# Kernel optimization log

Measured on AMD Instinct MI355X. Metric: run time of the kernel, lower is better.

The kernel has to match this reference:

```python
import jax, jax.numpy as jnp
import numpy as np

B, SEQ, DIM = 2, 2048, 1024
HEADS, HEAD_DIM = 16, 64
HIDDEN = 2816
EPS = 1e-5
LN_EPS = 1e-5


def rmsnorm(x, w, eps=EPS):
    return x * jax.lax.rsqrt(jnp.mean(x * x, axis=-1, keepdims=True) + eps) * w


def layernorm(x, w, b, eps=LN_EPS):
    mu = jnp.mean(x, axis=-1, keepdims=True)
    var = jnp.mean((x - mu) ** 2, axis=-1, keepdims=True)
    return (x - mu) * jax.lax.rsqrt(var + eps) * w + b


def modulate(x, shift, scale):
    # x: [B,S,D], shift/scale: [B,D]
    return x * (1.0 + scale[:, None, :]) + shift[:, None, :]


def apply_rope(t, cos, sin):
    # t: [B,S,H,D]; cos/sin: [S, D/2] -> complex multiply on (even,odd) pairs
    t = t.reshape(*t.shape[:-1], HEAD_DIM // 2, 2)
    t0, t1 = t[..., 0], t[..., 1]
    c = cos[None, :, None, :]
    s = sin[None, :, None, :]
    o0 = t0 * c - t1 * s
    o1 = t0 * s + t1 * c
    return jnp.stack([o0, o1], axis=-1).reshape(*t.shape[:-2], HEAD_DIM)


def setup_inputs() -> dict:
    key = jax.random.key(0)
    ks = jax.random.split(key, 12)
    def w(k, shape, s=0.02):
        return jax.random.normal(k, shape, dtype=jnp.float32) * s
    x = jax.random.normal(ks[0], (B, SEQ, DIM), dtype=jnp.float32)
    adaln_input = jax.random.normal(ks[1], (B, DIM), dtype=jnp.float32)
    pos = jnp.arange(SEQ, dtype=jnp.float32)
    inv_freq = 1.0 / (10000.0 ** (jnp.arange(0, HEAD_DIM, 2, dtype=jnp.float32) / HEAD_DIM))
    ang = pos[:, None] * inv_freq[None, :]  # [S, D/2]
    return dict(
        x=x, adaln_input=adaln_input,
        freqs_cos=jnp.cos(ang), freqs_sin=jnp.sin(ang),
        wq=w(ks[2], (DIM, DIM)), wk=w(ks[3], (DIM, DIM)),
        wv=w(ks[4], (DIM, DIM)), wo=w(ks[5], (DIM, DIM)),
        q_norm_w=jnp.ones(DIM, jnp.float32), q_norm_b=jnp.zeros(DIM, jnp.float32),
        k_norm_w=jnp.ones(DIM, jnp.float32), k_norm_b=jnp.zeros(DIM, jnp.float32),
        attn_norm_w=jnp.ones(DIM, jnp.float32), ffn_norm_w=jnp.ones(DIM, jnp.float32),
        ada_w=w(ks[6], (DIM, 6 * DIM)), ada_b=jnp.zeros(6 * DIM, jnp.float32),
        w1=w(ks[7], (DIM, HIDDEN)), w2=w(ks[8], (HIDDEN, DIM)), w3=w(ks[9], (DIM, HIDDEN)),
    )


def reference(x, adaln_input, freqs_cos, freqs_sin, wq, wk, wv, wo,
              q_norm_w, q_norm_b, k_norm_w, k_norm_b,
              attn_norm_w, ffn_norm_w, ada_w, ada_b, w1, w2, w3):
    # adaLN modulation: SiLU -> Linear -> 6 chunks of [B, DIM]
    m = jax.nn.silu(adaln_input) @ ada_w + ada_b
    shift_msa, scale_msa, gate_msa, shift_mlp, scale_mlp, gate_mlp = jnp.split(m, 6, axis=1)

    # --- attention branch ---
    h = modulate(rmsnorm(x, attn_norm_w), shift_msa, scale_msa)
    xq = layernorm(h @ wq, q_norm_w, q_norm_b)
    xk = layernorm(h @ wk, k_norm_w, k_norm_b)
    xv = h @ wv
    xq = xq.reshape(B, SEQ, HEADS, HEAD_DIM)
    xk = xk.reshape(B, SEQ, HEADS, HEAD_DIM)
    xv = xv.reshape(B, SEQ, HEADS, HEAD_DIM)
    xq = apply_rope(xq, freqs_cos, freqs_sin)
    xk = apply_rope(xk, freqs_cos, freqs_sin)
    scale = 1.0 / jnp.sqrt(jnp.float32(HEAD_DIM))
    scores = jnp.einsum('bshd,bthd->bhst', xq, xk) * scale  # [B,H,S,S]
    probs = jax.nn.softmax(scores, axis=-1)
    attn = jnp.einsum('bhst,bthd->bshd', probs, xv).reshape(B, SEQ, DIM)
    attn = attn @ wo
    x = x + gate_msa[:, None, :] * attn

    # --- MLP branch (SwiGLU) ---
    h = modulate(rmsnorm(x, ffn_norm_w), shift_mlp, scale_mlp)
    ffn = (jax.nn.silu(h @ w1) * (h @ w3)) @ w2
    x = x + gate_mlp[:, None, :] * ffn
    return x
```

## Files before the change

### kernel.cpp

```cpp
#include <hip/hip_runtime.h>
#include <hip/hip_bf16.h>

#define B_   2
#define S_   2048
#define D_   1024
#define H_   16
#define HD_  64
#define HID_ 2816

typedef unsigned short u16;
typedef unsigned int   u32;
typedef __attribute__((ext_vector_type(8))) short short8;
typedef __attribute__((ext_vector_type(4))) float f32x4;
typedef __attribute__((ext_vector_type(4))) u32   u32x4;

static __device__ __forceinline__ float bf2f(u16 u){ return __uint_as_float(((u32)u)<<16); }
static __device__ __forceinline__ u16 f2bf(float f){
  u32 u = __float_as_uint(f);
  u32 r = (u + 0x7FFFu + ((u>>16)&1u)) >> 16;
  return (u16)r;
}
static __device__ __forceinline__ u16 f2bfr(float f){
  return (u16)((__float_as_uint(f) + 0x8000u) >> 16);
}
static __device__ __forceinline__ u32 pk2(float a, float b){
  return ((__float_as_uint(a) + 0x8000u) >> 16) | ((__float_as_uint(b) + 0x8000u) & 0xFFFF0000u);
}

static __device__ __forceinline__ void ld4(const u16* p, float* v){
  ushort4 t = *reinterpret_cast<const ushort4*>(p);
  v[0]=bf2f(t.x); v[1]=bf2f(t.y); v[2]=bf2f(t.z); v[3]=bf2f(t.w);
}
static __device__ __forceinline__ void ld4(const float* p, float* v){
  float4 t = *reinterpret_cast<const float4*>(p);
  v[0]=t.x; v[1]=t.y; v[2]=t.z; v[3]=t.w;
}
static __device__ __forceinline__ void st4(u16* p, const float* v){
  ushort4 t; t.x=f2bf(v[0]); t.y=f2bf(v[1]); t.z=f2bf(v[2]); t.w=f2bf(v[3]);
  *reinterpret_cast<ushort4*>(p)=t;
}

static __device__ __forceinline__ float ld1g(const void* p, size_t i, bool f32){
  return f32 ? ((const float*)p)[i] : bf2f(((const u16*)p)[i]);
}
static __device__ __forceinline__ void ld4g(const void* p, size_t i, float* v, bool f32){
  if(f32){
    float4 t = *reinterpret_cast<const float4*>((const float*)p + i);
    v[0]=t.x; v[1]=t.y; v[2]=t.z; v[3]=t.w;
  }else{
    ushort4 t = *reinterpret_cast<const ushort4*>((const u16*)p + i);
    v[0]=bf2f(t.x); v[1]=bf2f(t.y); v[2]=bf2f(t.z); v[3]=bf2f(t.w);
  }
}
static __device__ __forceinline__ void st4g(void* p, size_t i, const float* v, bool f32){
  if(f32){
    float4 t; t.x=v[0]; t.y=v[1]; t.z=v[2]; t.w=v[3];
    *reinterpret_cast<float4*>((float*)p + i) = t;
  }else{
    st4((u16*)p + i, v);
  }
}

static __device__ __forceinline__ void gl2lds16(const u16* g, const u16* l){
  typedef __attribute__((address_space(3))) u16 lds_u16;
  typedef const __attribute__((address_space(1))) u16 glb_u16;
  __builtin_amdgcn_global_load_lds((glb_u16*)(uintptr_t)g,
                                   (lds_u16*)(u32)(uintptr_t)l, 16, 0, 0);
}

__global__ __launch_bounds__(256) void k_probe_zero(const u16* fc_raw, int* flag, float* m){
  int i = blockIdx.x*256 + threadIdx.x;
  if(i < 12288) m[i] = 0.f;
  if(i == 0) *flag = (fc_raw[0]==0) ? 1 : 0;
}

static __device__ __forceinline__ float blk_sum(float v, float* red){
  #pragma unroll
  for(int o=32;o;o>>=1) v += __shfl_xor(v,o,64);
  int lane = threadIdx.x & 63, w = threadIdx.x >> 6;
  if(lane==0) red[w]=v;
  __syncthreads();
  float t = red[0]+red[1]+red[2]+red[3];
  __syncthreads();
  return t;
}

__global__ __launch_bounds__(256) void k_adaln(const void* a, const void* W, const void* bias,
                                               float* m, const int* flag){
  bool f32 = flag[0] != 0;
  __shared__ float sl[2][128];
  int bk = blockIdx.y;
  {
    int bb = threadIdx.x >> 7, kk = threadIdx.x & 127;
    float x = ld1g(a, bb*D_ + bk*128 + kk, f32);
    sl[bb][kk] = x/(1.f+__expf(-x));
  }
  __syncthreads();
  int n = blockIdx.x*256 + threadIdx.x;
  float p0 = 0.f, p1 = 0.f;
  for(int kk=0;kk<128;kk++){
    float w = ld1g(W, (size_t)(bk*128+kk)*6144 + n, f32);
    p0 += sl[0][kk]*w; p1 += sl[1][kk]*w;
  }
  if(bk==0){ float bv = ld1g(bias, n, f32); p0 += bv; p1 += bv; }
  atomicAdd(&m[n], p0);
  atomicAdd(&m[6144+n], p1);
}

__global__ __launch_bounds__(256) void k_rms_mod(const void* x, const void* nw, const float* m,
                                                 u16* h, int shift_off, int scale_off,
                                                 const int* flag){
  bool f32 = flag[0] != 0;
  __shared__ float red[4];
  int row = blockIdx.x; int b = row >> 11;
  int d0 = threadIdx.x*4;
  float v[4]; ld4g(x, (size_t)row*D_ + d0, v, f32);
  float ss = v[0]*v[0]+v[1]*v[1]+v[2]*v[2]+v[3]*v[3];
  float tot = blk_sum(ss, red);
  float r = rsqrtf(tot*(1.f/D_) + 1e-5f);
  const float* mb = m + b*6144;
  float wn[4]; ld4g(nw, d0, wn, f32);
  float o[4];
  #pragma unroll
  for(int j=0;j<4;j++){
    int d = d0+j;
    o[j] = v[j]*r*wn[j]*(1.f+mb[scale_off+d]) + mb[shift_off+d];
  }
  st4(h + (size_t)row*D_ + d0, o);
}

__global__ __launch_bounds__(256) void k_resid_rms(const void* x, const u16* y, const float* m,
                                                   const void* nw, float* x2, u16* h,
                                                   const int* flag){
  bool f32 = flag[0] != 0;
  __shared__ float red[4];
  int row = blockIdx.x; int b = row >> 11;
  int d0 = threadIdx.x*4;
  size_t i4 = (size_t)row*D_ + d0;
  float xv[4], yv[4];
  ld4g(x, i4, xv, f32); ld4(y+i4, yv);
  const float* mb = m + b*6144;
  float v[4];
  #pragma unroll
  for(int j=0;j<4;j++) v[j] = xv[j] + mb[2048+d0+j]*yv[j];
  float4 t; t.x=v[0]; t.y=v[1]; t.z=v[2]; t.w=v[3];
  *reinterpret_cast<float4*>(x2+i4) = t;
  float ss = v[0]*v[0]+v[1]*v[1]+v[2]*v[2]+v[3]*v[3];
  float tot = blk_sum(ss, red);
  float r = rsqrtf(tot*(1.f/D_) + 1e-5f);
  float wn[4]; ld4g(nw, d0, wn, f32);
  float o[4];
  #pragma unroll
  for(int j=0;j<4;j++)
    o[j] = v[j]*r*wn[j]*(1.f+mb[4096+d0+j]) + mb[3072+d0+j];
  st4(h + i4, o);
}

__global__ __launch_bounds__(256) void k_ln_rope2(u16* t, const void* qw, const void* qb,
                                                  const void* kw, const void* kb2,
                                                  const void* fc, const void* fs, const int* flag){
  bool f32 = flag[0] != 0;
  __shared__ float red[4];
  int row = blockIdx.x; int s = row & (S_-1);
  const void* w  = blockIdx.y ? kw  : qw;
  const void* bb = blockIdx.y ? kb2 : qb;
  int d0 = threadIdx.x*4;
  u16* tp = t + (size_t)row*3072 + blockIdx.y*1024 + d0;
  float v[4]; ld4(tp, v);
  float sm = v[0]+v[1]+v[2]+v[3];
  float sq = v[0]*v[0]+v[1]*v[1]+v[2]*v[2]+v[3]*v[3];
  float tsm = blk_sum(sm, red);
  float tsq = blk_sum(sq, red);
  float mu  = tsm*(1.f/D_);
  float var = tsq*(1.f/D_) - mu*mu;
  float rs  = rsqrtf(var + 1e-5f);
  float wv[4], bv[4]; ld4g(w, d0, wv, f32); ld4g(bb, d0, bv, f32);
  float y[4];
  #pragma unroll
  for(int j=0;j<4;j++) y[j] = (v[j]-mu)*rs*wv[j] + bv[j];
  int pos = d0 & 63; int i0 = pos>>1;
  float c0 = ld1g(fc, s*32+i0,   f32), s0 = ld1g(fs, s*32+i0,   f32);
  float c1 = ld1g(fc, s*32+i0+1, f32), s1 = ld1g(fs, s*32+i0+1, f32);
  float o[4];
  o[0] = y[0]*c0 - y[1]*s0;
  o[1] = y[0]*s0 + y[1]*c0;
  o[2] = y[2]*c1 - y[3]*s1;
  o[3] = y[2]*s1 + y[3]*c1;
  st4(tp, o);
}

__global__ __launch_bounds__(256) void k_wt3(const void* W0, const void* W1, const void* W2,
                                             u16* WT, int Kd, int Nd, const int* flag){
  bool f32 = flag[0] != 0;
  const void* W = blockIdx.z==0 ? W0 : (blockIdx.z==1 ? W1 : W2);
  u16* dst_base = WT + (size_t)blockIdx.z * (size_t)Kd * Nd;
  __shared__ u16 L[64][72];
  int tid = threadIdx.x;
  int k0 = blockIdx.x*64, n0 = blockIdx.y*64;
  int r = tid>>2, c0 = (tid&3)*16;
  if(f32){
    const float* Wf = (const float*)W;
    #pragma unroll
    for(int j=0;j<4;j++){
      float4 t = *reinterpret_cast<const float4*>(&Wf[(size_t)(k0+r)*Nd + n0 + c0 + j*4]);
      L[r][c0+j*4+0]=f2bfr(t.x); L[r][c0+j*4+1]=f2bfr(t.y);
      L[r][c0+j*4+2]=f2bfr(t.z); L[r][c0+j*4+3]=f2bfr(t.w);
    }
  }else{
    const u16* Wh = (const u16*)W;
    *reinterpret_cast<short8*>(&L[r][c0]) =
      *reinterpret_cast<const short8*>(&Wh[(size_t)(k0+r)*Nd + n0 + c0]);
    *reinterpret_cast<short8*>(&L[r][c0+8]) =
      *reinterpret_cast<const short8*>(&Wh[(size_t)(k0+r)*Nd + n0 + c0 + 8]);
  }
  __syncthreads();
  int n = tid>>2, kk0 = (tid&3)*16;
  u16 tmp[16];
  #pragma unroll
  for(int j=0;j<16;j++) tmp[j] = L[kk0+j][n];
  u16* dst = dst_base + (size_t)(n0+n)*Kd + k0 + kk0;
  *reinterpret_cast<short8*>(dst)   = *reinterpret_cast<const short8*>(tmp);
  *reinterpret_cast<short8*>(dst+8) = *reinterpret_cast<const short8*>(tmp+8);
}

template<int TM>
__global__ __launch_bounds__(256) void k_gemm_mfma(const u16* A, int lda, const u16* BT, int ldb,
                                                   u16* C, int M, int N, int K){
  __shared__ __align__(16) u16 As[TM*64];
  __shared__ __align__(16) u16 Bs[128*64];
  int tid = threadIdx.x, lane = tid&63, w = tid>>6;
  int col = lane&15, quad = lane>>4;
  int row0 = blockIdx.y*TM, col0 = blockIdx.x*128;
  const u16* Ab = A  + (size_t)row0*lda;
  const u16* Bb = BT + (size_t)col0*ldb;
  constexpr int MI = TM/32;
  int wm = (w>>1)*(TM/2);
  int wn = (w&1)*64;
  f32x4 acc[MI][4];
  #pragma unroll
  for(int i=0;i<MI;i++)
    #pragma unroll
    for(int j=0;j<4;j++) acc[i][j] = (f32x4){0.f,0.f,0.f,0.f};

  for(int k0=0;k0<K;k0+=64){
    __syncthreads();
    #pragma unroll
    for(int i=0;i<TM/32;i++){
      int c = i*256 + w*64 + lane;
      int r = c>>3, s = c&7, gs = s ^ (r&7);
      gl2lds16(Ab + (size_t)r*lda + k0 + gs*8, As + (size_t)c*8);
    }
    #pragma unroll
    for(int i=0;i<4;i++){
      int c = i*256 + w*64 + lane;
      int r = c>>3, s = c&7, gs = s ^ (r&7);
      gl2lds16(Bb + (size_t)r*ldb + k0 + gs*8, Bs + (size_t)c*8);
    }
    __syncthreads();
    #pragma unroll
    for(int ks=0;ks<64;ks+=32){
      short8 af[MI], bfr[4];
      #pragma unroll
      for(int mi=0;mi<MI;mi++){
        int r = wm+mi*16+col;
        int sch = ((ks>>3) + quad) ^ (col&7);
        af[mi] = *reinterpret_cast<const short8*>(&As[r*64 + sch*8]);
      }
      #pragma unroll
      for(int ni=0;ni<4;ni++){
        int r = wn+ni*16+col;
        int sch = ((ks>>3) + quad) ^ (col&7);
        bfr[ni] = *reinterpret_cast<const short8*>(&Bs[r*64 + sch*8]);
      }
      #pragma unroll
      for(int mi=0;mi<MI;mi++)
        #pragma unroll
        for(int ni=0;ni<4;ni++)
          acc[mi][ni] = __builtin_amdgcn_mfma_f32_16x16x32_bf16(af[mi], bfr[ni], acc[mi][ni], 0,0,0);
    }
  }
  #pragma unroll
  for(int mi=0;mi<MI;mi++)
    #pragma unroll
    for(int r=0;r<4;r++){
      size_t rowoff = (size_t)(row0+wm+mi*16+quad*4+r)*N + col0 + wn;
      #pragma unroll
      for(int ni=0;ni<4;ni++)
        C[rowoff + ni*16 + col] = f2bfr(acc[mi][ni][r]);
    }
}

__global__ __launch_bounds__(256) void k_vt(const u16* v, int vstr, u16* vt){
  __shared__ u16 L[64][72];
  int tid = threadIdx.x;
  int wg = blockIdx.x;
  int kblk = wg & 31; int bh = wg >> 5; int h = bh & 15, b = bh >> 4;
  int row = tid>>2, c0 = (tid&3)*16;
  const u16* src = v + (size_t)(b*S_ + kblk*64 + row)*vstr + h*HD_ + c0;
  *reinterpret_cast<short8*>(&L[row][c0])   = *reinterpret_cast<const short8*>(src);
  *reinterpret_cast<short8*>(&L[row][c0+8]) = *reinterpret_cast<const short8*>(src+8);
  __syncthreads();
  int hd = tid>>2, k0 = (tid&3)*16;
  u16 tmp[16];
  #pragma unroll
  for(int j=0;j<16;j++) tmp[j] = L[k0+j][hd];
  u16* dst = vt + ((size_t)bh*HD_ + hd)*S_ + kblk*64 + k0;
  *reinterpret_cast<short8*>(dst)   = *reinterpret_cast<const short8*>(tmp);
  *reinterpret_cast<short8*>(dst+8) = *reinterpret_cast<const short8*>(tmp+8);
}

__global__ __launch_bounds__(256) void k_attn_mfma(const u16* q, const u16* k, const u16* vt,
                                                   u16* o, int qks){
  __shared__ __align__(16) u16 Ks[64*88];
  __shared__ __align__(16) u16 Vs[64*88];
  int tid = threadIdx.x, lane = tid & 63, wid = tid >> 6;
  int col = lane & 15, quad = lane >> 4;
  int wg = blockIdx.x;
  int qblk = wg & 31; int bh = wg >> 5; int h = bh & 15, b = bh >> 4;

  const u16* kb  = k  + (size_t)b*S_*qks + h*HD_;
  const u16* vtb = vt + (size_t)bh*HD_*S_;

  short8 qa0, qa1;
  {
    const float qscale = 0.18033688f;
    const u16* qp = q + (size_t)(b*S_ + qblk*64 + wid*16 + col)*qks + h*HD_ + quad*8;
    short8 t0 = *reinterpret_cast<const short8*>(qp);
    short8 t1 = *reinterpret_cast<const short8*>(qp + 32);
    #pragma unroll
    for(int j=0;j<8;j++){
      qa0[j] = (short)f2bf(bf2f((u16)t0[j])*qscale);
      qa1[j] = (short)f2bf(bf2f((u16)t1[j])*qscale);
    }
  }
  float m_i = -1e30f, l_i = 0.f;
  f32x4 acc[4];
  #pragma unroll
  for(int t=0;t<4;t++) acc[t] = (f32x4){0.f,0.f,0.f,0.f};

  const u16 *kp[2]; const u16 *vp[2]; u16 *ksd[2], *vsd[2];
  #pragma unroll
  for(int g=0;g<2;g++){
    int c = g*256 + tid;
    int l = c>>3, kc = (c&7)*8;
    int kl = 32*(l>>5) + 8*((l>>2)&3) + 4*((l>>4)&1) + (l&3);
    kp[g]  = kb + (size_t)kl*qks + kc;
    vp[g]  = vtb + (size_t)l*S_ + kc;
    ksd[g] = Ks + l*88 + kc;
    vsd[g] = Vs + l*88 + kc;
  }

  for(int t0=0;t0<S_;t0+=64){
    __syncthreads();
    #pragma unroll
    for(int g=0;g<2;g++){
      *reinterpret_cast<short8*>(ksd[g]) =
        *reinterpret_cast<const short8*>(kp[g] + (size_t)t0*qks);
      *reinterpret_cast<short8*>(vsd[g]) =
        *reinterpret_cast<const short8*>(vp[g] + t0);
    }
    __syncthreads();

    f32x4 st[4];
    #pragma unroll
    for(int mt=0;mt<4;mt++){
      st[mt] = (f32x4){0.f,0.f,0.f,0.f};
      short8 ka0 = *reinterpret_cast<const short8*>(&Ks[(mt*16+col)*88 + quad*8]);
      short8 ka1 = *reinterpret_cast<const short8*>(&Ks[(mt*16+col)*88 + 32 + quad*8]);
      st[mt] = __builtin_amdgcn_mfma_f32_16x16x32_bf16(ka0, qa0, st[mt], 0,0,0);
      st[mt] = __builtin_amdgcn_mfma_f32_16x16x32_bf16(ka1, qa1, st[mt], 0,0,0);
    }
    float cm = st[0][0];
    #pragma unroll
    for(int mt=0;mt<4;mt++)
      #pragma unroll
      for(int r=0;r<4;r++) cm = fmaxf(cm, st[mt][r]);
    cm = fmaxf(cm, __shfl_xor(cm,16,64));
    cm = fmaxf(cm, __shfl_xor(cm,32,64));
    float mn = fmaxf(m_i, cm);
    float al = __builtin_amdgcn_exp2f(m_i - mn);
    m_i = mn;
    float pe[4][4];
    #pragma unroll
    for(int mt=0;mt<4;mt++)
      #pragma unroll
      for(int r=0;r<4;r++) pe[mt][r] = __builtin_amdgcn_exp2f(st[mt][r]-mn);
    #pragma unroll
    for(int t=0;t<4;t++) acc[t] *= al;
    #pragma unroll
    for(int w=0;w<2;w++){
      u32x4 pw;
      pw[0] = pk2(pe[2*w][0],   pe[2*w][1]);
      pw[1] = pk2(pe[2*w][2],   pe[2*w][3]);
      pw[2] = pk2(pe[2*w+1][0], pe[2*w+1][1]);
      pw[3] = pk2(pe[2*w+1][2], pe[2*w+1][3]);
      short8 pb = *reinterpret_cast<short8*>(&pw);
      #pragma unroll
      for(int ht=0;ht<4;ht++){
        short8 vf = *reinterpret_cast<const short8*>(&Vs[(ht*16+col)*88 + w*32 + quad*8]);
        acc[ht] = __builtin_amdgcn_mfma_f32_16x16x32_bf16(vf, pb, acc[ht], 0,0,0);
      }
    }
    float ps = 0.f;
    #pragma unroll
    for(int mt=0;mt<4;mt++)
      #pragma unroll
      for(int r=0;r<4;r++) ps += pe[mt][r];
    ps += __shfl_xor(ps,16,64);
    ps += __shfl_xor(ps,32,64);
    l_i = l_i*al + ps;
  }
  float inv = __builtin_amdgcn_rcpf(l_i);
  u16* ob = o + (size_t)(b*S_ + qblk*64 + wid*16 + col)*D_ + h*HD_;
  #pragma unroll
  for(int ht=0;ht<4;ht++){
    uint2 t;
    t.x = pk2(acc[ht][0]*inv, acc[ht][1]*inv);
    t.y = pk2(acc[ht][2]*inv, acc[ht][3]*inv);
    *reinterpret_cast<uint2*>(ob + ht*16 + quad*4) = t;
  }
}

__global__ __launch_bounds__(256) void k_resid_b(const float* x, const u16* y, const float* m,
                                                 int gate_off, void* o, const int* flag){
  bool f32 = flag[0] != 0;
  size_t i4 = ((size_t)blockIdx.x*256 + threadIdx.x)*4;
  int d = (int)(i4 & (D_-1));
  int b = (int)(i4 >> 21);
  float xv[4], yv[4];
  ld4(x+i4, xv); ld4(y+i4, yv);
  const float* g = m + b*6144 + gate_off + d;
  float r[4];
  #pragma unroll
  for(int j=0;j<4;j++) r[j] = xv[j] + g[j]*yv[j];
  st4g(o, i4, r, f32);
}

__global__ __launch_bounds__(256) void k_silu_mul(u16* h13){
  int c4 = (blockIdx.x*256 + threadIdx.x)*4;
  if(c4 >= HID_) return;
  u16* p = h13 + (size_t)blockIdx.y*5632 + c4;
  float a[4], c[4];
  ld4(p, a); ld4(p + HID_, c);
  float r[4];
  #pragma unroll
  for(int j=0;j<4;j++){ float sv = a[j]/(1.f+__expf(-a[j])); r[j] = sv*c[j]; }
  st4(p, r);
}

extern "C" void kernel_launch(void* const* d_in, const int* in_sizes, int n_in,
                              void* d_out, int out_size, void* d_ws, size_t ws_size,
                              hipStream_t stream){
  const void* x   = d_in[0];
  const void* ada = d_in[1];
  const void* fc  = d_in[2];
  const void* fs  = d_in[3];
  const void* wq  = d_in[4];
  const void* wk  = d_in[5];
  const void* wv  = d_in[6];
  const void* wo  = d_in[7];
  const void* qnw = d_in[8];
  const void* qnb = d_in[9];
  const void* knw = d_in[10];
  const void* knb = d_in[11];
  const void* anw = d_in[12];
  const void* fnw = d_in[13];
  const void* aw  = d_in[14];
  const void* ab  = d_in[15];
  const void* w1  = d_in[16];
  const void* w2  = d_in[17];
  const void* w3  = d_in[18];
  char* ws = (char*)d_ws;
  const size_t MB = 1u<<20;

  int*   flag = (int*)ws;
  float* m    = (float*)(ws + 4096);
  u16*  hbuf  = (u16*)(ws + 1*MB);
  u16*  xqkv  = (u16*)(ws + 9*MB);
  float* x2   = (float*)(ws + 9*MB);
  u16*  proj  = (u16*)(ws + 25*MB);
  u16*  wreg  = (u16*)(ws + 33*MB);
  u16*  h13   = (u16*)(ws + 45*MB);
  u16*  vt    = wreg;

  dim3 blk(256);

  k_probe_zero<<<dim3(48), blk, 0, stream>>>((const u16*)fc, flag, m);
  k_adaln<<<dim3(24,8), blk, 0, stream>>>(ada, aw, ab, m, flag);
  k_rms_mod<<<dim3(B_*S_), blk, 0, stream>>>(x, anw, m, hbuf, 0, 1024, flag);

  k_wt3<<<dim3(16,16,3), blk, 0, stream>>>(wq, wk, wv, wreg, 1024, 1024, flag);
  k_gemm_mfma<128><<<dim3(24,32), blk, 0, stream>>>(hbuf, 1024, wreg, 1024, xqkv, 4096, 3072, 1024);

  k_ln_rope2<<<dim3(B_*S_,2), blk, 0, stream>>>(xqkv, qnw, qnb, knw, knb, fc, fs, flag);
  k_vt<<<dim3(B_*H_*S_/64), blk, 0, stream>>>(xqkv + 2048, 3072, vt);
  k_attn_mfma<<<dim3(B_*H_*S_/64), blk, 0, stream>>>(xqkv, xqkv + 1024, vt, hbuf, 3072);

  k_wt3<<<dim3(16,16,1), blk, 0, stream>>>(wo, wo, wo, wreg, 1024, 1024, flag);
  k_gemm_mfma<64><<<dim3(8,64), blk, 0, stream>>>(hbuf, 1024, wreg, 1024, proj, 4096, 1024, 1024);
  k_resid_rms<<<dim3(B_*S_), blk, 0, stream>>>(x, proj, m, fnw, x2, hbuf, flag);

  k_wt3<<<dim3(16,44,2), blk, 0, stream>>>(w1, w3, w3, wreg, 1024, 2816, flag);
  k_gemm_mfma<128><<<dim3(44,32), blk, 0, stream>>>(hbuf, 1024, wreg, 1024, h13, 4096, 5632, 1024);
  k_silu_mul<<<dim3(3,4096), blk, 0, stream>>>(h13);
  k_wt3<<<dim3(44,16,1), blk, 0, stream>>>(w2, w2, w2, wreg, 2816, 1024, flag);
  k_gemm_mfma<64><<<dim3(8,64), blk, 0, stream>>>(h13, 5632, wreg, 2816, proj, 4096, 1024, 2816);
  k_resid_b<<<dim3(4096), blk, 0, stream>>>(x2, proj, m, 5120, d_out, flag);
}
```

Baseline: 457.1 us.

## Fuse SwiGLU and residual into GEMM epilogues, double-buffer attention K/V tiles

The w1/w3 weights are now interleaved in 32-column groups so each GEMM tile holds matching gate and up columns, and the SiLU-multiply runs in the GEMM epilogue. That removes the separate silu_mul kernel and halves the intermediate writes. The final w2 GEMM now applies the gated residual directly in its epilogue, replacing k_resid_b and the proj round-trip. Attention gains double-buffered K/V shared tiles with register prefetch, a smaller row stride, and rescaling that is skipped when the running max is unchanged, which adds a warp-uniform branch.

Measured after the change: 441.8 us. -3.4%, faster.

```diff
diff --git a/kernel.cpp b/kernel.cpp
--- a/kernel.cpp
+++ b/kernel.cpp
@@ -223,9 +223,48 @@
   *reinterpret_cast<short8*>(dst+8) = *reinterpret_cast<const short8*>(tmp+8);
 }
 
-template<int TM>
+__global__ __launch_bounds__(256) void k_wt13(const void* W1, const void* W3,
+                                              u16* WT, const int* flag){
+  bool f32 = flag[0] != 0;
+  const int Kd = 1024, Nd = HID_;
+  const void* W = blockIdx.z ? W3 : W1;
+  int radd = blockIdx.z ? 32 : 0;
+  __shared__ u16 L[64][72];
+  int tid = threadIdx.x;
+  int k0 = blockIdx.x*64, n0 = blockIdx.y*64;
+  int r = tid>>2, c0 = (tid&3)*16;
+  if(f32){
+    const float* Wf = (const float*)W;
+    #pragma unroll
+    for(int j=0;j<4;j++){
+      float4 t = *reinterpret_cast<const float4*>(&Wf[(size_t)(k0+r)*Nd + n0 + c0 + j*4]);
+      L[r][c0+j*4+0]=f2bfr(t.x); L[r][c0+j*4+1]=f2bfr(t.y);
+      L[r][c0+j*4+2]=f2bfr(t.z); L[r][c0+j*4+3]=f2bfr(t.w);
+    }
+  }else{
+    const u16* Wh = (const u16*)W;
+    *reinterpret_cast<short8*>(&L[r][c0]) =
+      *reinterpret_cast<const short8*>(&Wh[(size_t)(k0+r)*Nd + n0 + c0]);
+    *reinterpret_cast<short8*>(&L[r][c0+8]) =
+      *reinterpret_cast<const short8*>(&Wh[(size_t)(k0+r)*Nd + n0 + c0 + 8]);
+  }
+  __syncthreads();
+  int n = tid>>2, kk0 = (tid&3)*16;
+  u16 tmp[16];
+  #pragma unroll
+  for(int j=0;j<16;j++) tmp[j] = L[kk0+j][n];
+  int nglob = n0 + n;
+  int rw = ((nglob>>5)<<6) + (nglob&31) + radd;
+  u16* dst = WT + (size_t)rw*Kd + k0 + kk0;
+  *reinterpret_cast<short8*>(dst)   = *reinterpret_cast<const short8*>(tmp);
+  *reinterpret_cast<short8*>(dst+8) = *reinterpret_cast<const short8*>(tmp+8);
+}
+
+template<int TM, int EPI>
 __global__ __launch_bounds__(256) void k_gemm_mfma(const u16* A, int lda, const u16* BT, int ldb,
-                                                   u16* C, int M, int N, int K){
+                                                   u16* C, int N, int K,
+                                                   const float* x2, const float* mg,
+                                                   void* outp, const int* flag){
   __shared__ __align__(16) u16 As[TM*64];
   __shared__ __align__(16) u16 Bs[128*64];
   int tid = threadIdx.x, lane = tid&63, w = tid>>6;
@@ -279,15 +318,48 @@
           acc[mi][ni] = __builtin_amdgcn_mfma_f32_16x16x32_bf16(af[mi], bfr[ni], acc[mi][ni], 0,0,0);
     }
   }
-  #pragma unroll
-  for(int mi=0;mi<MI;mi++)
-    #pragma unroll
-    for(int r=0;r<4;r++){
-      size_t rowoff = (size_t)(row0+wm+mi*16+quad*4+r)*N + col0 + wn;
-      #pragma unroll
-      for(int ni=0;ni<4;ni++)
-        C[rowoff + ni*16 + col] = f2bfr(acc[mi][ni][r]);
-    }
+  if constexpr(EPI==0){
+    #pragma unroll
+    for(int mi=0;mi<MI;mi++)
+      #pragma unroll
+      for(int r=0;r<4;r++){
+        size_t rowoff = (size_t)(row0+wm+mi*16+quad*4+r)*N + col0 + wn;
+        #pragma unroll
+        for(int ni=0;ni<4;ni++)
+          C[rowoff + ni*16 + col] = f2bfr(acc[mi][ni][r]);
+      }
+  } else if constexpr(EPI==1){
+    int cb = blockIdx.x*64 + (wn?32:0) + col;
+    #pragma unroll
+    for(int mi=0;mi<MI;mi++)
+      #pragma unroll
+      for(int r=0;r<4;r++){
+        int row = row0+wm+mi*16+quad*4+r;
+        u16* gp = C + (size_t)row*HID_ + cb;
+        #pragma unroll
+        for(int ni=0;ni<2;ni++){
+          float a = acc[mi][ni][r], cc = acc[mi][ni+2][r];
+          float sv = a * __builtin_amdgcn_rcpf(1.f + __builtin_amdgcn_exp2f(-1.4426950f*a));
+          gp[ni*16] = f2bfr(sv*cc);
+        }
+      }
+  } else {
+    bool f32o = flag[0] != 0;
+    #pragma unroll
+    for(int mi=0;mi<MI;mi++)
+      #pragma unroll
+      for(int r=0;r<4;r++){
+        int row = row0+wm+mi*16+quad*4+r;
+        int b = row >> 11;
+        #pragma unroll
+        for(int ni=0;ni<4;ni++){
+          int cc = col0 + wn + ni*16 + col;
+          float v = x2[(size_t)row*D_ + cc] + mg[b*6144 + 5120 + cc]*acc[mi][ni][r];
+          if(f32o) ((float*)outp)[(size_t)row*D_ + cc] = v;
+          else     ((u16*)outp)[(size_t)row*D_ + cc]   = f2bfr(v);
+        }
+      }
+  }
 }
 
 __global__ __launch_bounds__(256) void k_vt(const u16* v, int vstr, u16* vt){
@@ -311,8 +383,8 @@
 
 __global__ __launch_bounds__(256) void k_attn_mfma(const u16* q, const u16* k, const u16* vt,
                                                    u16* o, int qks){
-  __shared__ __align__(16) u16 Ks[64*88];
-  __shared__ __align__(16) u16 Vs[64*88];
+  __shared__ __align__(16) u16 Ks[2][64*72];
+  __shared__ __align__(16) u16 Vs[2][64*72];
   int tid = threadIdx.x, lane = tid & 63, wid = tid >> 6;
   int col = lane & 15, quad = lane >> 4;
   int wg = blockIdx.x;
@@ -338,35 +410,43 @@
   #pragma unroll
   for(int t=0;t<4;t++) acc[t] = (f32x4){0.f,0.f,0.f,0.f};
 
-  const u16 *kp[2]; const u16 *vp[2]; u16 *ksd[2], *vsd[2];
-  #pragma unroll
-  for(int g=0;g<2;g++){
-    int c = g*256 + tid;
-    int l = c>>3, kc = (c&7)*8;
-    int kl = 32*(l>>5) + 8*((l>>2)&3) + 4*((l>>4)&1) + (l&3);
-    kp[g]  = kb + (size_t)kl*qks + kc;
-    vp[g]  = vtb + (size_t)l*S_ + kc;
-    ksd[g] = Ks + l*88 + kc;
-    vsd[g] = Vs + l*88 + kc;
-  }
-
-  for(int t0=0;t0<S_;t0+=64){
+  int l0 = tid>>3,        kc0 = (tid&7)*8;
+  int l1 = (256+tid)>>3,  kc1 = ((256+tid)&7)*8;
+  int kl0 = 32*(l0>>5) + 8*((l0>>2)&3) + 4*((l0>>4)&1) + (l0&3);
+  int kl1 = 32*(l1>>5) + 8*((l1>>2)&3) + 4*((l1>>4)&1) + (l1&3);
+  const u16* kp0 = kb + (size_t)kl0*qks + kc0;
+  const u16* kp1 = kb + (size_t)kl1*qks + kc1;
+  const u16* vp0 = vtb + (size_t)l0*S_ + kc0;
+  const u16* vp1 = vtb + (size_t)l1*S_ + kc1;
+  int ko0 = l0*72 + kc0, ko1 = l1*72 + kc1;
+
+  {
+    *reinterpret_cast<short8*>(&Ks[0][ko0]) = *reinterpret_cast<const short8*>(kp0);
+    *reinterpret_cast<short8*>(&Ks[0][ko1]) = *reinterpret_cast<const short8*>(kp1);
+    *reinterpret_cast<short8*>(&Vs[0][ko0]) = *reinterpret_cast<const short8*>(vp0);
+    *reinterpret_cast<short8*>(&Vs[0][ko1]) = *reinterpret_cast<const short8*>(vp1);
+  }
+
+  for(int i=0;i<32;i++){
     __syncthreads();
-    #pragma unroll
-    for(int g=0;g<2;g++){
-      *reinterpret_cast<short8*>(ksd[g]) =
-        *reinterpret_cast<const short8*>(kp[g] + (size_t)t0*qks);
-      *reinterpret_cast<short8*>(vsd[g]) =
-        *reinterpret_cast<const short8*>(vp[g] + t0);
-    }
-    __syncthreads();
+    const u16* Kc = Ks[i&1];
+    const u16* Vc = Vs[i&1];
+    short8 nk0, nk1, nv0, nv1;
+    bool more = (i < 31);
+    if(more){
+      size_t t0n = (size_t)(i+1)*64;
+      nk0 = *reinterpret_cast<const short8*>(kp0 + t0n*qks);
+      nk1 = *reinterpret_cast<const short8*>(kp1 + t0n*qks);
+      nv0 = *reinterpret_cast<const short8*>(vp0 + t0n);
+      nv1 = *reinterpret_cast<const short8*>(vp1 + t0n);
+    }
 
     f32x4 st[4];
     #pragma unroll
     for(int mt=0;mt<4;mt++){
       st[mt] = (f32x4){0.f,0.f,0.f,0.f};
-      short8 ka0 = *reinterpret_cast<const short8*>(&Ks[(mt*16+col)*88 + quad*8]);
-      short8 ka1 = *reinterpret_cast<const short8*>(&Ks[(mt*16+col)*88 + 32 + quad*8]);
+      short8 ka0 = *reinterpret_cast<const short8*>(&Kc[(mt*16+col)*72 + quad*8]);
+      short8 ka1 = *reinterpret_cast<const short8*>(&Kc[(mt*16+col)*72 + 32 + quad*8]);
       st[mt] = __builtin_amdgcn_mfma_f32_16x16x32_bf16(ka0, qa0, st[mt], 0,0,0);
       st[mt] = __builtin_amdgcn_mfma_f32_16x16x32_bf16(ka1, qa1, st[mt], 0,0,0);
     }
@@ -377,16 +457,19 @@
       for(int r=0;r<4;r++) cm = fmaxf(cm, st[mt][r]);
     cm = fmaxf(cm, __shfl_xor(cm,16,64));
     cm = fmaxf(cm, __shfl_xor(cm,32,64));
-    float mn = fmaxf(m_i, cm);
-    float al = __builtin_amdgcn_exp2f(m_i - mn);
-    m_i = mn;
+    if(__any(cm > m_i)){
+      float mn = fmaxf(m_i, cm);
+      float al = __builtin_amdgcn_exp2f(m_i - mn);
+      m_i = mn;
+      l_i *= al;
+      #pragma unroll
+      for(int t=0;t<4;t++) acc[t] *= al;
+    }
     float pe[4][4];
     #pragma unroll
     for(int mt=0;mt<4;mt++)
       #pragma unroll
-      for(int r=0;r<4;r++) pe[mt][r] = __builtin_amdgcn_exp2f(st[mt][r]-mn);
-    #pragma unroll
-    for(int t=0;t<4;t++) acc[t] *= al;
+      for(int r=0;r<4;r++) pe[mt][r] = __builtin_amdgcn_exp2f(st[mt][r]-m_i);
     #pragma unroll
     for(int w=0;w<2;w++){
       u32x4 pw;
@@ -397,7 +480,7 @@
       short8 pb = *reinterpret_cast<short8*>(&pw);
       #pragma unroll
       for(int ht=0;ht<4;ht++){
-        short8 vf = *reinterpret_cast<const short8*>(&Vs[(ht*16+col)*88 + w*32 + quad*8]);
+        short8 vf = *reinterpret_cast<const short8*>(&Vc[(ht*16+col)*72 + w*32 + quad*8]);
         acc[ht] = __builtin_amdgcn_mfma_f32_16x16x32_bf16(vf, pb, acc[ht], 0,0,0);
       }
     }
@@ -408,7 +491,16 @@
       for(int r=0;r<4;r++) ps += pe[mt][r];
     ps += __shfl_xor(ps,16,64);
     ps += __shfl_xor(ps,32,64);
-    l_i = l_i*al + ps;
+    l_i += ps;
+
+    if(more){
+      u16* Kn = (u16*)Ks[(i+1)&1];
+      u16* Vn = (u16*)Vs[(i+1)&1];
+      *reinterpret_cast<short8*>(&Kn[ko0]) = nk0;
+      *reinterpret_cast<short8*>(&Kn[ko1]) = nk1;
+      *reinterpret_cast<short8*>(&Vn[ko0]) = nv0;
+      *reinterpret_cast<short8*>(&Vn[ko1]) = nv1;
+    }
   }
   float inv = __builtin_amdgcn_rcpf(l_i);
   u16* ob = o + (size_t)(b*S_ + qblk*64 + wid*16 + col)*D_ + h*HD_;
@@ -419,33 +511,6 @@
     t.y = pk2(acc[ht][2]*inv, acc[ht][3]*inv);
     *reinterpret_cast<uint2*>(ob + ht*16 + quad*4) = t;
   }
-}
-
-__global__ __launch_bounds__(256) void k_resid_b(const float* x, const u16* y, const float* m,
-                                                 int gate_off, void* o, const int* flag){
-  bool f32 = flag[0] != 0;
-  size_t i4 = ((size_t)blockIdx.x*256 + threadIdx.x)*4;
-  int d = (int)(i4 & (D_-1));
-  int b = (int)(i4 >> 21);
-  float xv[4], yv[4];
-  ld4(x+i4, xv); ld4(y+i4, yv);
-  const float* g = m + b*6144 + gate_off + d;
-  float r[4];
-  #pragma unroll
-  for(int j=0;j<4;j++) r[j] = xv[j] + g[j]*yv[j];
-  st4g(o, i4, r, f32);
-}
-
-__global__ __launch_bounds__(256) void k_silu_mul(u16* h13){
-  int c4 = (blockIdx.x*256 + threadIdx.x)*4;
-  if(c4 >= HID_) return;
-  u16* p = h13 + (size_t)blockIdx.y*5632 + c4;
-  float a[4], c[4];
-  ld4(p, a); ld4(p + HID_, c);
-  float r[4];
-  #pragma unroll
-  for(int j=0;j<4;j++){ float sv = a[j]/(1.f+__expf(-a[j])); r[j] = sv*c[j]; }
-  st4(p, r);
 }
 
 extern "C" void kernel_launch(void* const* d_in, const int* in_sizes, int n_in,
@@ -480,7 +545,7 @@
   float* x2   = (float*)(ws + 9*MB);
   u16*  proj  = (u16*)(ws + 25*MB);
   u16*  wreg  = (u16*)(ws + 33*MB);
-  u16*  h13   = (u16*)(ws + 45*MB);
+  u16*  g     = (u16*)(ws + 45*MB);
   u16*  vt    = wreg;
 
   dim3 blk(256);
@@ -490,20 +555,22 @@
   k_rms_mod<<<dim3(B_*S_), blk, 0, stream>>>(x, anw, m, hbuf, 0, 1024, flag);
 
   k_wt3<<<dim3(16,16,3), blk, 0, stream>>>(wq, wk, wv, wreg, 1024, 1024, flag);
-  k_gemm_mfma<128><<<dim3(24,32), blk, 0, stream>>>(hbuf, 1024, wreg, 1024, xqkv, 4096, 3072, 1024);
+  k_gemm_mfma<128,0><<<dim3(24,32), blk, 0, stream>>>(hbuf, 1024, wreg, 1024, xqkv,
+                                                      3072, 1024, nullptr, nullptr, nullptr, flag);
 
   k_ln_rope2<<<dim3(B_*S_,2), blk, 0, stream>>>(xqkv, qnw, qnb, knw, knb, fc, fs, flag);
   k_vt<<<dim3(B_*H_*S_/64), blk, 0, stream>>>(xqkv + 2048, 3072, vt);
   k_attn_mfma<<<dim3(B_*H_*S_/64), blk, 0, stream>>>(xqkv, xqkv + 1024, vt, hbuf, 3072);
 
   k_wt3<<<dim3(16,16,1), blk, 0, stream>>>(wo, wo, wo, wreg, 1024, 1024, flag);
-  k_gemm_mfma<64><<<dim3(8,64), blk, 0, stream>>>(hbuf, 1024, wreg, 1024, proj, 4096, 1024, 1024);
+  k_gemm_mfma<64,0><<<dim3(8,64), blk, 0, stream>>>(hbuf, 1024, wreg, 1024, proj,
+                                                    1024, 1024, nullptr, nullptr, nullptr, flag);
   k_resid_rms<<<dim3(B_*S_), blk, 0, stream>>>(x, proj, m, fnw, x2, hbuf, flag);
 
-  k_wt3<<<dim3(16,44,2), blk, 0, stream>>>(w1, w3, w3, wreg, 1024, 2816, flag);
-  k_gemm_mfma<128><<<dim3(44,32), blk, 0, stream>>>(hbuf, 1024, wreg, 1024, h13, 4096, 5632, 1024);
-  k_silu_mul<<<dim3(3,4096), blk, 0, stream>>>(h13);
+  k_wt13<<<dim3(16,44,2), blk, 0, stream>>>(w1, w3, wreg, flag);
+  k_gemm_mfma<128,1><<<dim3(44,32), blk, 0, stream>>>(hbuf, 1024, wreg, 1024, g,
+                                                      5632, 1024, nullptr, nullptr, nullptr, flag);
   k_wt3<<<dim3(44,16,1), blk, 0, stream>>>(w2, w2, w2, wreg, 2816, 1024, flag);
-  k_gemm_mfma<64><<<dim3(8,64), blk, 0, stream>>>(h13, 5632, wreg, 2816, proj, 4096, 1024, 2816);
-  k_resid_b<<<dim3(4096), blk, 0, stream>>>(x2, proj, m, 5120, d_out, flag);
-}
+  k_gemm_mfma<64,2><<<dim3(8,64), blk, 0, stream>>>(g, 2816, wreg, 2816, nullptr,
+                                                    1024, 2816, x2, m, d_out, flag);
+}
```
